# Performance work log

Measured on AMD Instinct MI355X. Metric: run time of the kernel, lower is better.

## Reference

```python
import jax, jax.numpy as jnp
import numpy as np

B, D, H, L = 4096, 8192, 4096, 128


def binarize_ste(v, thresh):
    # BinarizeTensorThresh with straight-through gradient (identity backward)
    return v + jax.lax.stop_gradient((v > thresh).astype(v.dtype) - v)


def setup_inputs() -> dict:
    key = jax.random.key(0)
    k0, k1, k2, k3 = jax.random.split(key, 4)
    x = (jax.random.uniform(k0, (B, D), jnp.float32) < 0.1).astype(jnp.float32)  # sparse binary data
    enc_weight = jax.random.normal(k1, (H, D), jnp.float32) * (2.0 / (H + D)) ** 0.5 + 0.5  # xavier-ish around binarize thresh
    bias0 = -jax.random.uniform(k2, (H,), jnp.float32)  # clipBias keeps bias <= 0
    bias3 = jnp.zeros((D,), jnp.float32)  # act3.noBias()
    clf_weight = jax.random.uniform(k3, (L, H), jnp.float32)  # clamped to [0,1]
    return {"x": x, "enc_weight": enc_weight, "bias0": bias0, "bias3": bias3, "clf_weight": clf_weight}


def reference(x, enc_weight, bias0, bias3, clf_weight):
    wb = binarize_ste(enc_weight, 0.5)                 # [H, D] binarized encoder weights
    h = jnp.einsum('bd,hd->bh', x, wb)                 # fc0_enc
    z = binarize_ste(h + bias0, 1.0)                   # act0: BinaryActivation (STE threshold)
    classification = jnp.einsum('bh,lh->bl', z, clf_weight)  # classifier (no bias)
    recon = jnp.einsum('bh,hd->bd', z, wb)             # fc3_dec: tied transposed binarized weights
    output = binarize_ste(recon + bias3, 1.0)          # act3
    return output, classification, z
```

## Files before the change

kernel.cpp:

```cpp
#include <hip/hip_runtime.h>
#include <cstdint>

typedef unsigned long long u64;

constexpr int B = 4096;
constexpr int D = 8192;
constexpr int H = 4096;
constexpr int L = 128;
constexpr int DW = D / 64;
constexpr int HW = H / 64;

__global__ __launch_bounds__(256) void k_pack(const float* __restrict__ x,
                                              const float* __restrict__ e,
                                              u64* __restrict__ xp,
                                              u64* __restrict__ wbpw) {
    int r = blockIdx.x;
    int lane = threadIdx.x & 63;
    int wave = threadIdx.x >> 6;
    bool is_x = (r < B);
    const float* row = is_x ? (x + (size_t)r * D) : (e + (size_t)(r - B) * D);
    #pragma unroll 1
    for (int it = 0; it < 8; ++it) {
        int chunk = wave * 8 + it;
        int base = chunk * 256;
        u64 m[4];
        #pragma unroll
        for (int k = 0; k < 4; ++k) {
            float v = row[base + k * 64 + lane];
            m[k] = __ballot(v > 0.5f);
        }
        if (lane == 0) {
            if (is_x) {
                u64* orow = xp + (size_t)r * DW + chunk * 4;
                orow[0] = m[0]; orow[1] = m[1]; orow[2] = m[2]; orow[3] = m[3];
            } else {
                int h = r - B;
                #pragma unroll
                for (int k = 0; k < 4; ++k)
                    wbpw[(size_t)(chunk * 4 + k) * H + h] = m[k];
            }
        }
    }
}

__global__ __launch_bounds__(256) void k_build_wbt(const u64* __restrict__ wbpw,
                                                   u64* __restrict__ wbtp) {
    int wid = (blockIdx.x * 256 + threadIdx.x) >> 6;
    int lane = threadIdx.x & 63;
    int dblock = wid >> 6;
    int wh = wid & (HW - 1);
    u64 Wj = wbpw[(size_t)dblock * H + wh * 64 + lane];
    u64 myword = 0;
    #pragma unroll 1
    for (int jj = 0; jj < 64; ++jj) {
        u64 m = __ballot((int)((Wj >> jj) & 1ull));
        if (lane == jj) myword = m;
    }
    wbtp[(size_t)(dblock * 64 + lane) * HW + wh] = myword;
}


__global__ void k_base(const u64* __restrict__ wbtp, const float* __restrict__ bias3,
                       float* __restrict__ base) {
    int d = blockIdx.x * blockDim.x + threadIdx.x;
    int s = 0;
    for (int w = 0; w < HW; ++w) s += (int)__popcll(wbtp[(size_t)d * HW + w]);
    base[d] = ((float)s + bias3[d] > 1.0f) ? 1.0f : 0.0f;
}

__global__ void k_cmin(const float* __restrict__ bias0, int* __restrict__ cmin) {
    int h = blockIdx.x * blockDim.x + threadIdx.x;
    float b0 = bias0[h];
    int c = (int)(1.0f - b0);
    if (c < 0) c = 0;
    int guard = 0;
    while ((float)c + b0 <= 1.0f && guard++ < 100000) ++c;
    while (c > 0 && (float)(c - 1) + b0 > 1.0f) --c;
    cmin[h] = c;
}

__global__ void k_rowsum(const float* __restrict__ clf, float* __restrict__ R) {
    __shared__ float s[256];
    int l = blockIdx.x;
    float acc = 0.f;
    for (int h = threadIdx.x; h < H; h += 256) acc += clf[(size_t)l * H + h];
    s[threadIdx.x] = acc;
    __syncthreads();
    for (int off = 128; off > 0; off >>= 1) {
        if ((int)threadIdx.x < off) s[threadIdx.x] += s[threadIdx.x + off];
        __syncthreads();
    }
    if (threadIdx.x == 0) R[l] = s[0];
}

__global__ __launch_bounds__(256) void k_z(const u64* __restrict__ xp,
                                           const u64* __restrict__ wbpw,
                                           const int* __restrict__ cmin,
                                           float* __restrict__ zout,
                                           u64* __restrict__ zp) {
    int wid0 = (blockIdx.x * 256 + threadIdx.x) >> 6;
    int lane = threadIdx.x & 63;
    int nwaves = gridDim.x * 4;
    #pragma unroll 1
    for (int pair = wid0; pair < B * HW; pair += nwaves) {
        int b = pair >> 6;
        int hb = pair & (HW - 1);
        int h = hb * 64 + lane;
        int cm = cmin[h];
        int cnt = 0;
        const u64* __restrict__ xr = xp + (size_t)b * DW;
        #pragma unroll 1
        for (int w = 0; w < DW; ++w) {
            if (__all(cnt >= cm)) break;
            if (cnt < cm) {
                u64 a = xr[w];
                u64 wv = wbpw[(size_t)w * H + h];
                cnt += (int)__popcll(a & wv);
            }
        }
        int zb = (cnt >= cm) ? 1 : 0;
        zout[(size_t)b * H + h] = zb ? 1.0f : 0.0f;
        u64 m = __ballot(zb);
        if (lane == 0) zp[(size_t)b * HW + hb] = m;
    }
}

__global__ void k_nz(const u64* __restrict__ zp, int* __restrict__ nz) {
    int b = blockIdx.x * blockDim.x + threadIdx.x;
    int s = 0;
    for (int w = 0; w < HW; ++w) s += (int)__popcll(zp[(size_t)b * HW + w]);
    nz[b] = H - s;
}


__global__ __launch_bounds__(256) void k_cls(const u64* __restrict__ zp,
                                             const float* __restrict__ R,
                                             const float* __restrict__ clf,
                                             const int* __restrict__ nz,
                                             float* __restrict__ out1) {
    int b = blockIdx.x * 2 + (threadIdx.x >> 7);
    int l = threadIdx.x & (L - 1);
    if (nz[b] == 0) {
        out1[(size_t)b * L + l] = R[l];
        return;
    }
    float acc = 0.f;
    for (int wh = 0; wh < HW; ++wh) {
        u64 m = zp[(size_t)b * HW + wh];
        while (m) {
            int j = __ffsll(m) - 1;
            acc += clf[(size_t)l * H + wh * 64 + j];
            m &= m - 1;
        }
    }
    out1[(size_t)b * L + l] = acc;
}

__global__ __launch_bounds__(256) void k_out(const float4* __restrict__ base4,
                                             const int* __restrict__ nz,
                                             const u64* __restrict__ zp,
                                             const u64* __restrict__ wbtp,
                                             const float* __restrict__ bias3,
                                             float* __restrict__ out0) {
    int nf4 = B * D / 4;
    int stride = gridDim.x * 256;
    #pragma unroll 1
    for (int t = blockIdx.x * 256 + threadIdx.x; t < nf4; t += stride) {
        int idx = t * 4;
        int b = idx >> 13;
        int d = idx & (D - 1);
        if (nz[b] == 0) {
            ((float4*)out0)[t] = base4[d >> 2];
        } else {
            const u64* __restrict__ zr = zp + (size_t)b * HW;
            for (int k = 0; k < 4; ++k) {
                int dd = d + k;
                int s = 0;
                for (int w = 0; w < HW; ++w)
                    s += (int)__popcll(zr[w] & wbtp[(size_t)dd * HW + w]);
                out0[(size_t)idx + k] = ((float)s + bias3[dd] > 1.0f) ? 1.0f : 0.0f;
            }
        }
    }
}


extern "C" void kernel_launch(void* const* d_in, const int* in_sizes, int n_in,
                              void* d_out, int out_size, void* d_ws, size_t ws_size,
                              hipStream_t stream) {
    const float* x   = (const float*)d_in[0];
    const float* ew  = (const float*)d_in[1];
    const float* b0  = (const float*)d_in[2];
    const float* b3  = (const float*)d_in[3];
    const float* clf = (const float*)d_in[4];

    float* out0 = (float*)d_out;
    float* out1 = out0 + (size_t)B * D;
    float* zout = out1 + (size_t)B * L;

    char* ws = (char*)d_ws;
    u64* xp    = (u64*)(ws);
    u64* wbpw  = (u64*)(ws + (4ull << 20));
    u64* wbtp  = (u64*)(ws + (8ull << 20));
    u64* zp    = (u64*)(ws + (12ull << 20));
    float* base = (float*)(ws + 14680064ull);
    float* R    = (float*)(ws + 14712832ull);
    int* cmin   = (int*)(ws + 14713344ull);
    int* nz     = (int*)(ws + 14729728ull);

    k_pack<<<B + H, 256, 0, stream>>>(x, ew, xp, wbpw);
    k_build_wbt<<<(DW * HW * 64) / 256, 256, 0, stream>>>(wbpw, wbtp);
    k_base<<<D / 256, 256, 0, stream>>>(wbtp, b3, base);
    k_cmin<<<H / 256, 256, 0, stream>>>(b0, cmin);
    k_rowsum<<<L, 256, 0, stream>>>(clf, R);
    k_z<<<8192, 256, 0, stream>>>(xp, wbpw, cmin, zout, zp);
    k_nz<<<B / 256, 256, 0, stream>>>(zp, nz);
    k_cls<<<B / 2, 256, 0, stream>>>(zp, R, clf, nz, out1);
    k_out<<<8192, 256, 0, stream>>>((const float4*)base, nz, zp, wbtp, b3, out0);
}
```

Baseline: 469.7 us.

## Fuse nine launches into three kernels with per-row z, classifier and decode

The pack, cmin and rowsum kernels are merged into one launch using block-index ranges. The transpose and base-row kernels are merged, and the base row is now computed from ballots instead of from the transposed matrix. The z, nz, classifier and output kernels become a single per-batch-row kernel that keeps the z bitmask in shared memory, which removes the zp/nz global round trips and six launch gaps. The cost is that the z computation is now one block per row with fixed work per wave, so the grid-stride balancing of the old kernel is lost.

```diff
diff --git a/kernel.cpp b/kernel.cpp
--- a/kernel.cpp
+++ b/kernel.cpp
@@ -10,105 +10,133 @@
 constexpr int DW = D / 64;
 constexpr int HW = H / 64;
 
-__global__ __launch_bounds__(256) void k_pack(const float* __restrict__ x,
-                                              const float* __restrict__ e,
-                                              u64* __restrict__ xp,
-                                              u64* __restrict__ wbpw) {
+__global__ __launch_bounds__(256) void k_A(const float* __restrict__ x,
+                                           const float* __restrict__ e,
+                                           const float* __restrict__ bias0,
+                                           const float* __restrict__ clf,
+                                           u64* __restrict__ xp,
+                                           u64* __restrict__ wbpw,
+                                           int* __restrict__ cmin,
+                                           float* __restrict__ R) {
+    __shared__ float s[256];
     int r = blockIdx.x;
     int lane = threadIdx.x & 63;
     int wave = threadIdx.x >> 6;
-    bool is_x = (r < B);
-    const float* row = is_x ? (x + (size_t)r * D) : (e + (size_t)(r - B) * D);
+
+    if (r < B + H) {
+        bool is_x = (r < B);
+        const float* row = is_x ? (x + (size_t)r * D) : (e + (size_t)(r - B) * D);
+        #pragma unroll 1
+        for (int it = 0; it < 8; ++it) {
+            int chunk = wave * 8 + it;
+            int base = chunk * 256;
+            u64 m[4];
+            #pragma unroll
+            for (int k = 0; k < 4; ++k) {
+                float v = row[base + k * 64 + lane];
+                m[k] = __ballot(v > 0.5f);
+            }
+            if (lane == 0) {
+                if (is_x) {
+                    u64* orow = xp + (size_t)r * DW + chunk * 4;
+                    orow[0] = m[0]; orow[1] = m[1]; orow[2] = m[2]; orow[3] = m[3];
+                } else {
+                    int h = r - B;
+                    #pragma unroll
+                    for (int k = 0; k < 4; ++k)
+                        wbpw[(size_t)(chunk * 4 + k) * H + h] = m[k];
+                }
+            }
+        }
+    } else if (r < B + H + 16) {
+        int h = (r - B - H) * 256 + threadIdx.x;
+        float b0 = bias0[h];
+        int c = (int)(1.0f - b0);
+        if (c < 0) c = 0;
+        int guard = 0;
+        while ((float)c + b0 <= 1.0f && guard++ < 100000) ++c;
+        while (c > 0 && (float)(c - 1) + b0 > 1.0f) --c;
+        cmin[h] = c;
+    } else {
+        int l = r - (B + H + 16);
+        float acc = 0.f;
+        for (int h = threadIdx.x; h < H; h += 256) acc += clf[(size_t)l * H + h];
+        s[threadIdx.x] = acc;
+        __syncthreads();
+        for (int off = 128; off > 0; off >>= 1) {
+            if ((int)threadIdx.x < off) s[threadIdx.x] += s[threadIdx.x + off];
+            __syncthreads();
+        }
+        if (threadIdx.x == 0) R[l] = s[0];
+    }
+}
+
+__global__ __launch_bounds__(256) void k_TB(const u64* __restrict__ wbpw,
+                                            const float* __restrict__ bias3,
+                                            u64* __restrict__ wbtp,
+                                            float* __restrict__ basef) {
+    int r = blockIdx.x;
+    int lane = threadIdx.x & 63;
+    int wave = threadIdx.x >> 6;
+    if (r < 2048) {
+        int wid = r * 4 + wave;
+        int dblock = wid >> 6;
+        int wh = wid & (HW - 1);
+        u64 Wj = wbpw[(size_t)dblock * H + wh * 64 + lane];
+        u64 myword = 0;
+        #pragma unroll 1
+        for (int jj = 0; jj < 64; ++jj) {
+            u64 m = __ballot((int)((Wj >> jj) & 1ull));
+            if (lane == jj) myword = m;
+        }
+        wbtp[(size_t)(dblock * 64 + lane) * HW + wh] = myword;
+    } else {
+        int w = r - 2048;
+        __shared__ int sc[4][64];
+        int cnt = 0;
+        #pragma unroll 1
+        for (int g = wave; g < 64; g += 4) {
+            u64 W = wbpw[(size_t)w * H + g * 64 + lane];
+            #pragma unroll 1
+            for (int jj = 0; jj < 64; ++jj) {
+                u64 m = __ballot((int)((W >> jj) & 1ull));
+                if (lane == jj) cnt += (int)__popcll(m);
+            }
+        }
+        sc[wave][lane] = cnt;
+        __syncthreads();
+        if (wave == 0) {
+            int tot = sc[0][lane] + sc[1][lane] + sc[2][lane] + sc[3][lane];
+            int d = w * 64 + lane;
+            basef[d] = ((float)tot + bias3[d] > 1.0f) ? 1.0f : 0.0f;
+        }
+    }
+}
+
+__global__ __launch_bounds__(256) void k_Z(const u64* __restrict__ xp,
+                                           const u64* __restrict__ wbpw,
+                                           const u64* __restrict__ wbtp,
+                                           const int* __restrict__ cmin,
+                                           const float* __restrict__ basef,
+                                           const float* __restrict__ R,
+                                           const float* __restrict__ clf,
+                                           const float* __restrict__ bias3,
+                                           float* __restrict__ out0,
+                                           float* __restrict__ out1,
+                                           float* __restrict__ zout) {
+    __shared__ u64 zrow[HW];
+    __shared__ int s_nz;
+    int b = blockIdx.x;
+    int lane = threadIdx.x & 63;
+    int wave = threadIdx.x >> 6;
+    const u64* __restrict__ xr = xp + (size_t)b * DW;
+
     #pragma unroll 1
-    for (int it = 0; it < 8; ++it) {
-        int chunk = wave * 8 + it;
-        int base = chunk * 256;
-        u64 m[4];
-        #pragma unroll
-        for (int k = 0; k < 4; ++k) {
-            float v = row[base + k * 64 + lane];
-            m[k] = __ballot(v > 0.5f);
-        }
-        if (lane == 0) {
-            if (is_x) {
-                u64* orow = xp + (size_t)r * DW + chunk * 4;
-                orow[0] = m[0]; orow[1] = m[1]; orow[2] = m[2]; orow[3] = m[3];
-            } else {
-                int h = r - B;
-                #pragma unroll
-                for (int k = 0; k < 4; ++k)
-                    wbpw[(size_t)(chunk * 4 + k) * H + h] = m[k];
-            }
-        }
-    }
-}
-
-__global__ __launch_bounds__(256) void k_build_wbt(const u64* __restrict__ wbpw,
-                                                   u64* __restrict__ wbtp) {
-    int wid = (blockIdx.x * 256 + threadIdx.x) >> 6;
-    int lane = threadIdx.x & 63;
-    int dblock = wid >> 6;
-    int wh = wid & (HW - 1);
-    u64 Wj = wbpw[(size_t)dblock * H + wh * 64 + lane];
-    u64 myword = 0;
-    #pragma unroll 1
-    for (int jj = 0; jj < 64; ++jj) {
-        u64 m = __ballot((int)((Wj >> jj) & 1ull));
-        if (lane == jj) myword = m;
-    }
-    wbtp[(size_t)(dblock * 64 + lane) * HW + wh] = myword;
-}
-
-
-__global__ void k_base(const u64* __restrict__ wbtp, const float* __restrict__ bias3,
-                       float* __restrict__ base) {
-    int d = blockIdx.x * blockDim.x + threadIdx.x;
-    int s = 0;
-    for (int w = 0; w < HW; ++w) s += (int)__popcll(wbtp[(size_t)d * HW + w]);
-    base[d] = ((float)s + bias3[d] > 1.0f) ? 1.0f : 0.0f;
-}
-
-__global__ void k_cmin(const float* __restrict__ bias0, int* __restrict__ cmin) {
-    int h = blockIdx.x * blockDim.x + threadIdx.x;
-    float b0 = bias0[h];
-    int c = (int)(1.0f - b0);
-    if (c < 0) c = 0;
-    int guard = 0;
-    while ((float)c + b0 <= 1.0f && guard++ < 100000) ++c;
-    while (c > 0 && (float)(c - 1) + b0 > 1.0f) --c;
-    cmin[h] = c;
-}
-
-__global__ void k_rowsum(const float* __restrict__ clf, float* __restrict__ R) {
-    __shared__ float s[256];
-    int l = blockIdx.x;
-    float acc = 0.f;
-    for (int h = threadIdx.x; h < H; h += 256) acc += clf[(size_t)l * H + h];
-    s[threadIdx.x] = acc;
-    __syncthreads();
-    for (int off = 128; off > 0; off >>= 1) {
-        if ((int)threadIdx.x < off) s[threadIdx.x] += s[threadIdx.x + off];
-        __syncthreads();
-    }
-    if (threadIdx.x == 0) R[l] = s[0];
-}
-
-__global__ __launch_bounds__(256) void k_z(const u64* __restrict__ xp,
-                                           const u64* __restrict__ wbpw,
-                                           const int* __restrict__ cmin,
-                                           float* __restrict__ zout,
-                                           u64* __restrict__ zp) {
-    int wid0 = (blockIdx.x * 256 + threadIdx.x) >> 6;
-    int lane = threadIdx.x & 63;
-    int nwaves = gridDim.x * 4;
-    #pragma unroll 1
-    for (int pair = wid0; pair < B * HW; pair += nwaves) {
-        int b = pair >> 6;
-        int hb = pair & (HW - 1);
+    for (int i = 0; i < HW / 4; ++i) {
+        int hb = wave * (HW / 4) + i;
         int h = hb * 64 + lane;
         int cm = cmin[h];
         int cnt = 0;
-        const u64* __restrict__ xr = xp + (size_t)b * DW;
         #pragma unroll 1
         for (int w = 0; w < DW; ++w) {
             if (__all(cnt >= cm)) break;
@@ -121,65 +149,44 @@
         int zb = (cnt >= cm) ? 1 : 0;
         zout[(size_t)b * H + h] = zb ? 1.0f : 0.0f;
         u64 m = __ballot(zb);
-        if (lane == 0) zp[(size_t)b * HW + hb] = m;
-    }
-}
-
-__global__ void k_nz(const u64* __restrict__ zp, int* __restrict__ nz) {
-    int b = blockIdx.x * blockDim.x + threadIdx.x;
-    int s = 0;
-    for (int w = 0; w < HW; ++w) s += (int)__popcll(zp[(size_t)b * HW + w]);
-    nz[b] = H - s;
-}
-
-
-__global__ __launch_bounds__(256) void k_cls(const u64* __restrict__ zp,
-                                             const float* __restrict__ R,
-                                             const float* __restrict__ clf,
-                                             const int* __restrict__ nz,
-                                             float* __restrict__ out1) {
-    int b = blockIdx.x * 2 + (threadIdx.x >> 7);
-    int l = threadIdx.x & (L - 1);
-    if (nz[b] == 0) {
-        out1[(size_t)b * L + l] = R[l];
-        return;
-    }
-    float acc = 0.f;
-    for (int wh = 0; wh < HW; ++wh) {
-        u64 m = zp[(size_t)b * HW + wh];
-        while (m) {
-            int j = __ffsll(m) - 1;
-            acc += clf[(size_t)l * H + wh * 64 + j];
-            m &= m - 1;
-        }
-    }
-    out1[(size_t)b * L + l] = acc;
-}
-
-__global__ __launch_bounds__(256) void k_out(const float4* __restrict__ base4,
-                                             const int* __restrict__ nz,
-                                             const u64* __restrict__ zp,
-                                             const u64* __restrict__ wbtp,
-                                             const float* __restrict__ bias3,
-                                             float* __restrict__ out0) {
-    int nf4 = B * D / 4;
-    int stride = gridDim.x * 256;
-    #pragma unroll 1
-    for (int t = blockIdx.x * 256 + threadIdx.x; t < nf4; t += stride) {
-        int idx = t * 4;
-        int b = idx >> 13;
-        int d = idx & (D - 1);
-        if (nz[b] == 0) {
-            ((float4*)out0)[t] = base4[d >> 2];
-        } else {
-            const u64* __restrict__ zr = zp + (size_t)b * HW;
-            for (int k = 0; k < 4; ++k) {
-                int dd = d + k;
-                int s = 0;
-                for (int w = 0; w < HW; ++w)
-                    s += (int)__popcll(zr[w] & wbtp[(size_t)dd * HW + w]);
-                out0[(size_t)idx + k] = ((float)s + bias3[dd] > 1.0f) ? 1.0f : 0.0f;
-            }
+        if (lane == 0) zrow[hb] = m;
+    }
+    __syncthreads();
+
+    if (wave == 0) {
+        int c = (int)__popcll(zrow[lane]);
+        #pragma unroll
+        for (int off = 32; off > 0; off >>= 1) c += __shfl_down(c, off);
+        if (lane == 0) s_nz = H - c;
+    }
+    __syncthreads();
+    int nz = s_nz;
+
+    if (nz == 0) {
+        if (threadIdx.x < L) out1[(size_t)b * L + threadIdx.x] = R[threadIdx.x];
+        float4* o4 = (float4*)(out0 + (size_t)b * D);
+        const float4* b4 = (const float4*)basef;
+        #pragma unroll
+        for (int t = threadIdx.x; t < D / 4; t += 256) o4[t] = b4[t];
+    } else {
+        if (threadIdx.x < L) {
+            int l = threadIdx.x;
+            float acc = 0.f;
+            for (int wh = 0; wh < HW; ++wh) {
+                u64 m = zrow[wh];
+                while (m) {
+                    int j = __ffsll(m) - 1;
+                    acc += clf[(size_t)l * H + wh * 64 + j];
+                    m &= m - 1;
+                }
+            }
+            out1[(size_t)b * L + l] = acc;
+        }
+        for (int d = threadIdx.x; d < D; d += 256) {
+            int ssum = 0;
+            for (int w = 0; w < HW; ++w)
+                ssum += (int)__popcll(zrow[w] & wbtp[(size_t)d * HW + w]);
+            out0[(size_t)b * D + d] = ((float)ssum + bias3[d] > 1.0f) ? 1.0f : 0.0f;
         }
     }
 }
@@ -199,22 +206,15 @@
     float* zout = out1 + (size_t)B * L;
 
     char* ws = (char*)d_ws;
-    u64* xp    = (u64*)(ws);
-    u64* wbpw  = (u64*)(ws + (4ull << 20));
-    u64* wbtp  = (u64*)(ws + (8ull << 20));
-    u64* zp    = (u64*)(ws + (12ull << 20));
-    float* base = (float*)(ws + 14680064ull);
-    float* R    = (float*)(ws + 14712832ull);
-    int* cmin   = (int*)(ws + 14713344ull);
-    int* nz     = (int*)(ws + 14729728ull);
-
-    k_pack<<<B + H, 256, 0, stream>>>(x, ew, xp, wbpw);
-    k_build_wbt<<<(DW * HW * 64) / 256, 256, 0, stream>>>(wbpw, wbtp);
-    k_base<<<D / 256, 256, 0, stream>>>(wbtp, b3, base);
-    k_cmin<<<H / 256, 256, 0, stream>>>(b0, cmin);
-    k_rowsum<<<L, 256, 0, stream>>>(clf, R);
-    k_z<<<8192, 256, 0, stream>>>(xp, wbpw, cmin, zout, zp);
-    k_nz<<<B / 256, 256, 0, stream>>>(zp, nz);
-    k_cls<<<B / 2, 256, 0, stream>>>(zp, R, clf, nz, out1);
-    k_out<<<8192, 256, 0, stream>>>((const float4*)base, nz, zp, wbtp, b3, out0);
-}
+    u64* xp     = (u64*)(ws);
+    u64* wbpw   = (u64*)(ws + (4ull << 20));
+    u64* wbtp   = (u64*)(ws + (8ull << 20));
+    float* basef = (float*)(ws + (12ull << 20));
+    float* R     = (float*)(ws + (12ull << 20) + 32768);
+    int* cmin    = (int*)(ws + (12ull << 20) + 32768 + 512);
+
+    k_A<<<B + H + 16 + L, 256, 0, stream>>>(x, ew, b0, clf, xp, wbpw, cmin, R);
+    k_TB<<<2048 + DW, 256, 0, stream>>>(wbpw, b3, wbtp, basef);
+    k_Z<<<B, 256, 0, stream>>>(xp, wbpw, wbtp, cmin, basef, R, clf, b3,
+                               out0, out1, zout);
+}
```

Measured after the change: 503.1 us. 7.1% more time.
